# Kernel optimization log

Measured on AMD Instinct MI355X. Metric: run time of the kernel, lower is better.

## Reference

```python
import jax, jax.numpy as jnp
import numpy as np

D_IN = 1024
D_OUT = 1024
B, S = 4, 4096


def setup_inputs() -> dict:
    key = jax.random.key(0)
    ks = jax.random.split(key, 7)
    scale = 1.0 / np.sqrt(D_IN)
    return {
        "x": jax.random.normal(ks[0], (B, S, D_IN), dtype=jnp.float32),
        "Wq": jax.random.uniform(ks[1], (D_IN, D_OUT), jnp.float32, -scale, scale),
        "bq": jax.random.uniform(ks[2], (D_OUT,), jnp.float32, -scale, scale),
        "Wk": jax.random.uniform(ks[3], (D_IN, D_OUT), jnp.float32, -scale, scale),
        "bk": jax.random.uniform(ks[4], (D_OUT,), jnp.float32, -scale, scale),
        "Wv": jax.random.uniform(ks[5], (D_IN, D_OUT), jnp.float32, -scale, scale),
        "bv": jax.random.uniform(ks[6], (D_OUT,), jnp.float32, -scale, scale),
    }


def reference(x, Wq, bq, Wk, bk, Wv, bv):
    # x: [B,S,d_in]
    q = jnp.einsum("bsd,de->bse", x, Wq) + bq  # [B,S,d_out]
    k = jnp.einsum("bsd,de->bse", x, Wk) + bk
    v = jnp.einsum("bsd,de->bse", x, Wv) + bv
    scores = jnp.einsum("bqe,bke->bqk", q, k) / jnp.sqrt(jnp.float32(D_OUT))  # [B,S,S]
    attn = jax.nn.softmax(scores, axis=2)
    return jnp.einsum("bqk,bke->bqe", attn, v)  # [B,S,d_out]
```

## Files before the change

kernel.cpp:

```cpp
#include <hip/hip_runtime.h>
#include <hip/hip_bf16.h>
#include <cstdint>

#define SEQ 4096
#define NB 4
#define DIM 1024
#define MTOT (NB * SEQ)
constexpr size_t EL = (size_t)MTOT * DIM;

using u16x8  = __attribute__((ext_vector_type(8))) unsigned short;
using bf16x8 = __attribute__((ext_vector_type(8))) __bf16;
using f32x4  = __attribute__((ext_vector_type(4))) float;

__device__ __forceinline__ unsigned short f2bf(float f) {
  return __builtin_bit_cast(unsigned short, __float2bfloat16(f));
}

__device__ __forceinline__ void gload16(const unsigned short* g, unsigned short* l) {
  __builtin_amdgcn_global_load_lds(
      (const __attribute__((address_space(1))) unsigned int*)g,
      (__attribute__((address_space(3))) unsigned int*)l, 16, 0, 0);
}
__device__ __forceinline__ void stage_half(const unsigned short* gsrc, size_t ld,
                                           unsigned short* ldst) {
  gload16(gsrc, ldst);
  gload16(gsrc + 64 * ld, ldst + 64 * 64);
}

#define BAR()   __builtin_amdgcn_s_barrier()
#define FENCE() asm volatile("" ::: "memory")

__global__ __launch_bounds__(256) void prep(const float* __restrict__ x,
                                            unsigned short* __restrict__ xb,
                                            const float* __restrict__ bq,
                                            const float* __restrict__ bk,
                                            const float* __restrict__ bv,
                                            float* __restrict__ bc,
                                            float* __restrict__ l) {
  const size_t gid = (size_t)blockIdx.x * 256 + threadIdx.x;
  const size_t i = gid * 4;
  float4 v = *(const float4*)(x + i);
  ushort4 o;
  o.x = f2bf(v.x); o.y = f2bf(v.y); o.z = f2bf(v.z); o.w = f2bf(v.w);
  *(ushort4*)(xb + i) = o;
  if (gid < MTOT) l[gid] = 0.f;
  if (gid < 3 * DIM)
    bc[gid] = gid < DIM ? bq[gid] : gid < 2 * DIM ? bk[gid - DIM] : bv[gid - 2 * DIM];
}

__global__ __launch_bounds__(256) void transpose_w3(const float* __restrict__ Wq,
                                                    const float* __restrict__ Wk,
                                                    const float* __restrict__ Wv,
                                                    unsigned short* __restrict__ WT) {
  const float* W = blockIdx.z == 0 ? Wq : blockIdx.z == 1 ? Wk : Wv;
  unsigned short* O = WT + (size_t)blockIdx.z * DIM * DIM;
  __shared__ float tile[32][33];
  const int tx = threadIdx.x, ty = threadIdx.y;
  const int d0 = blockIdx.y * 32, e0 = blockIdx.x * 32;
#pragma unroll
  for (int j = 0; j < 32; j += 8)
    tile[ty + j][tx] = W[(size_t)(d0 + ty + j) * DIM + e0 + tx];
  __syncthreads();
#pragma unroll
  for (int j = 0; j < 32; j += 8)
    O[(size_t)(e0 + ty + j) * DIM + d0 + tx] = f2bf(tile[tx][ty + j]);
}

enum { EPI_QKV = 0, EPI_EXP = 1, EPI_PV = 2 };

template <int EPI>
__device__ __forceinline__ void gemm_body(
    const unsigned short* __restrict__ A, const unsigned short* __restrict__ B,
    void* __restrict__ C, const float* __restrict__ bias, float* __restrict__ lsum,
    int K, int lda, int ldb, int ldc, float scale,
    int row0, int col0, int bz, long sA, long sB, long sC) {
  __shared__ unsigned short sm[2][2][256 * 64];
  const int t    = threadIdx.x;
  const int lane = t & 63;
  const int wave = t >> 6;
  const int wm   = wave >> 2;
  const int wn   = wave & 3;
  const int fr   = lane & 15;
  const int g    = lane >> 4;
  const int xr   = (fr & 7) << 4;

  const unsigned short* Ab = A + (size_t)bz * (size_t)sA;
  const unsigned short* Bb = B + (size_t)bz * (size_t)sB;

  const int srow = t >> 3;
  const int scol = ((((t & 7) << 4) ^ ((srow & 7) << 4)) >> 1);
  const unsigned short* gA = Ab + (size_t)(row0 + srow) * (size_t)lda + scol;
  const unsigned short* gB = Bb + (size_t)(col0 + srow) * (size_t)ldb + scol;

  const int arow = wm * 128 + fr;
  const int brow = wn * 64 + fr;
  const int c0 = (((g << 4)) ^ xr) >> 1;
  const int c1 = ((64 | (g << 4)) ^ xr) >> 1;

  f32x4 acc[8][4];
  const f32x4 z4 = {0.f, 0.f, 0.f, 0.f};
#pragma unroll
  for (int i = 0; i < 8; ++i)
#pragma unroll
    for (int j = 0; j < 4; ++j) acc[i][j] = z4;

  const int nt = K >> 6;

  stage_half(gA, lda, &sm[0][0][wave * 512]);
  stage_half(gA + 128 * (size_t)lda, lda, &sm[0][0][8192 + wave * 512]);
  stage_half(gB, ldb, &sm[0][1][wave * 512]);
  stage_half(gB + 128 * (size_t)ldb, ldb, &sm[0][1][8192 + wave * 512]);
  if (nt > 1) {
    stage_half(gB + 64, ldb, &sm[1][1][wave * 512]);
    stage_half(gB + 128 * (size_t)ldb + 64, ldb, &sm[1][1][8192 + wave * 512]);
    stage_half(gA + 64, lda, &sm[1][0][wave * 512]);
    asm volatile("s_waitcnt vmcnt(6)" ::: "memory");
  } else {
    asm volatile("s_waitcnt vmcnt(0)" ::: "memory");
  }
  BAR(); FENCE();

  bf16x8 a0[4][2], a1[4][2], b0[2][2], b1[2][2];

  for (int kt = 0; kt < nt; ++kt) {
    const int p = kt & 1;
    const unsigned short* As  = sm[p][0];
    const unsigned short* Bs2 = sm[p][1];

#pragma unroll
    for (int mi = 0; mi < 4; ++mi) {
      a0[mi][0] = *(const bf16x8*)(As + (arow + mi * 16) * 64 + c0);
      a0[mi][1] = *(const bf16x8*)(As + (arow + mi * 16) * 64 + c1);
    }
#pragma unroll
    for (int ni = 0; ni < 2; ++ni) {
      b0[ni][0] = *(const bf16x8*)(Bs2 + (brow + ni * 16) * 64 + c0);
      b0[ni][1] = *(const bf16x8*)(Bs2 + (brow + ni * 16) * 64 + c1);
    }
    if (kt + 1 < nt)
      stage_half(gA + 128 * (size_t)lda + (size_t)(kt + 1) * 64, lda,
                 &sm[p ^ 1][0][8192 + wave * 512]);
    FENCE(); BAR(); FENCE();
    __builtin_amdgcn_s_setprio(1);
#pragma unroll
    for (int mi = 0; mi < 4; ++mi)
#pragma unroll
      for (int ni = 0; ni < 2; ++ni) {
        acc[mi][ni] = __builtin_amdgcn_mfma_f32_16x16x32_bf16(a0[mi][0], b0[ni][0], acc[mi][ni], 0, 0, 0);
        acc[mi][ni] = __builtin_amdgcn_mfma_f32_16x16x32_bf16(a0[mi][1], b0[ni][1], acc[mi][ni], 0, 0, 0);
      }
    __builtin_amdgcn_s_setprio(0);
    FENCE(); BAR(); FENCE();

#pragma unroll
    for (int ni = 0; ni < 2; ++ni) {
      b1[ni][0] = *(const bf16x8*)(Bs2 + (brow + (ni + 2) * 16) * 64 + c0);
      b1[ni][1] = *(const bf16x8*)(Bs2 + (brow + (ni + 2) * 16) * 64 + c1);
    }
    FENCE(); BAR(); FENCE();
    __builtin_amdgcn_s_setprio(1);
#pragma unroll
    for (int mi = 0; mi < 4; ++mi)
#pragma unroll
      for (int ni = 0; ni < 2; ++ni) {
        acc[mi][ni + 2] = __builtin_amdgcn_mfma_f32_16x16x32_bf16(a0[mi][0], b1[ni][0], acc[mi][ni + 2], 0, 0, 0);
        acc[mi][ni + 2] = __builtin_amdgcn_mfma_f32_16x16x32_bf16(a0[mi][1], b1[ni][1], acc[mi][ni + 2], 0, 0, 0);
      }
    __builtin_amdgcn_s_setprio(0);
    FENCE(); BAR(); FENCE();

#pragma unroll
    for (int mi = 0; mi < 4; ++mi) {
      a1[mi][0] = *(const bf16x8*)(As + (arow + (mi + 4) * 16) * 64 + c0);
      a1[mi][1] = *(const bf16x8*)(As + (arow + (mi + 4) * 16) * 64 + c1);
    }
    if (kt + 2 < nt)
      stage_half(gB + (size_t)(kt + 2) * 64, ldb, &sm[p][1][wave * 512]);
    FENCE(); BAR(); FENCE();
    __builtin_amdgcn_s_setprio(1);
#pragma unroll
    for (int mi = 0; mi < 4; ++mi)
#pragma unroll
      for (int ni = 0; ni < 2; ++ni) {
        acc[mi + 4][ni] = __builtin_amdgcn_mfma_f32_16x16x32_bf16(a1[mi][0], b0[ni][0], acc[mi + 4][ni], 0, 0, 0);
        acc[mi + 4][ni] = __builtin_amdgcn_mfma_f32_16x16x32_bf16(a1[mi][1], b0[ni][1], acc[mi + 4][ni], 0, 0, 0);
      }
    __builtin_amdgcn_s_setprio(0);
    FENCE(); BAR(); FENCE();

    if (kt + 2 < nt) {
      stage_half(gB + 128 * (size_t)ldb + (size_t)(kt + 2) * 64, ldb,
                 &sm[p][1][8192 + wave * 512]);
      stage_half(gA + (size_t)(kt + 2) * 64, lda, &sm[p][0][wave * 512]);
      asm volatile("s_waitcnt vmcnt(6)" ::: "memory");
    } else {
      asm volatile("s_waitcnt vmcnt(0)" ::: "memory");
    }
    FENCE(); BAR(); FENCE();
    __builtin_amdgcn_s_setprio(1);
#pragma unroll
    for (int mi = 0; mi < 4; ++mi)
#pragma unroll
      for (int ni = 0; ni < 2; ++ni) {
        acc[mi + 4][ni + 2] = __builtin_amdgcn_mfma_f32_16x16x32_bf16(a1[mi][0], b1[ni][0], acc[mi + 4][ni + 2], 0, 0, 0);
        acc[mi + 4][ni + 2] = __builtin_amdgcn_mfma_f32_16x16x32_bf16(a1[mi][1], b1[ni][1], acc[mi + 4][ni + 2], 0, 0, 0);
      }
    __builtin_amdgcn_s_setprio(0);
    FENCE(); BAR(); FENCE();
  }

  char* Lb = (char*)&sm[0][0][0];
  const int rb = (lane >> 4) * 4;

  if constexpr (EPI == EPI_QKV) {
    const int which = col0 >> 10;
    const int lc0   = col0 & 1023;
    unsigned short* Co = (unsigned short*)C + (size_t)which * EL;
    if (which < 2) {
      float bb[4];
#pragma unroll
      for (int ni = 0; ni < 4; ++ni) bb[ni] = bias[col0 + wn * 64 + ni * 16 + fr];
#pragma unroll
      for (int mi = 0; mi < 8; ++mi) {
        const int r0 = wm * 128 + mi * 16 + rb;
#pragma unroll
        for (int ni = 0; ni < 4; ++ni) {
          const int c = wn * 64 + ni * 16 + fr;
#pragma unroll
          for (int j = 0; j < 4; ++j) {
            const int r = r0 + j;
            *(unsigned short*)(Lb + r * 512 + ((c * 2) ^ ((r & 7) << 4))) =
                f2bf(acc[mi][ni][j] + bb[ni]);
          }
        }
      }
      __syncthreads();
#pragma unroll 4
      for (int i = 0; i < 16; ++i) {
        const int G = i * 512 + t;
        const int r = G >> 5, c16 = G & 31;
        u16x8 v = *(const u16x8*)(Lb + r * 512 + ((c16 * 16) ^ ((r & 7) << 4)));
        *(u16x8*)(Co + (size_t)(row0 + r) * DIM + lc0 + c16 * 8) = v;
      }
    } else {
#pragma unroll
      for (int ni = 0; ni < 4; ++ni) {
        const int c = wn * 64 + ni * 16 + fr;
        const float bb = bias[col0 + c];
#pragma unroll
        for (int mi = 0; mi < 8; ++mi) {
          const int r0 = wm * 128 + mi * 16 + rb;
          ushort4 pk;
          pk.x = f2bf(acc[mi][ni][0] + bb);
          pk.y = f2bf(acc[mi][ni][1] + bb);
          pk.z = f2bf(acc[mi][ni][2] + bb);
          pk.w = f2bf(acc[mi][ni][3] + bb);
          *(ushort4*)(Lb + c * 512 + ((r0 * 2) ^ ((c & 7) << 4))) = pk;
        }
      }
      __syncthreads();
#pragma unroll 4
      for (int i = 0; i < 16; ++i) {
        const int G = i * 512 + t;
        const int e = G >> 5, m16 = G & 31;
        u16x8 v = *(const u16x8*)(Lb + e * 512 + ((m16 * 16) ^ ((e & 7) << 4)));
        *(u16x8*)(Co + (size_t)(lc0 + e) * MTOT + row0 + m16 * 8) = v;
      }
    }
  } else if constexpr (EPI == EPI_EXP) {
#pragma unroll
    for (int mi = 0; mi < 8; ++mi)
#pragma unroll
      for (int ni = 0; ni < 4; ++ni)
#pragma unroll
        for (int j = 0; j < 4; ++j)
          acc[mi][ni][j] = exp2f(acc[mi][ni][j] * scale);

#pragma unroll
    for (int mi = 0; mi < 8; ++mi)
#pragma unroll
      for (int j = 0; j < 4; ++j) {
        float s = acc[mi][0][j] + acc[mi][1][j] + acc[mi][2][j] + acc[mi][3][j];
        s += __shfl_xor(s, 1);
        s += __shfl_xor(s, 2);
        s += __shfl_xor(s, 4);
        s += __shfl_xor(s, 8);
        if (fr == 0)
          atomicAdd(&lsum[(size_t)bz * SEQ + row0 + wm * 128 + mi * 16 + rb + j], s);
      }

#pragma unroll
    for (int mi = 0; mi < 8; ++mi) {
      const int r0 = wm * 128 + mi * 16 + rb;
#pragma unroll
      for (int ni = 0; ni < 4; ++ni) {
        const int c = wn * 64 + ni * 16 + fr;
#pragma unroll
        for (int j = 0; j < 4; ++j) {
          const int r = r0 + j;
          *(unsigned short*)(Lb + r * 512 + ((c * 2) ^ ((r & 7) << 4))) =
              f2bf(acc[mi][ni][j]);
        }
      }
    }
    __syncthreads();
    unsigned short* Co = (unsigned short*)C + (size_t)bz * (size_t)sC;
#pragma unroll 4
    for (int i = 0; i < 16; ++i) {
      const int G = i * 512 + t;
      const int r = G >> 5, c16 = G & 31;
      u16x8 v = *(const u16x8*)(Lb + r * 512 + ((c16 * 16) ^ ((r & 7) << 4)));
      *(u16x8*)(Co + (size_t)(row0 + r) * (size_t)ldc + col0 + c16 * 8) = v;
    }
  } else {
    float* Co = (float*)C + (size_t)bz * (size_t)sC;
#pragma unroll
    for (int h = 0; h < 2; ++h) {
      if (h) __syncthreads();
      if (wm == h) {
#pragma unroll
        for (int mi = 0; mi < 8; ++mi) {
          const int r0 = mi * 16 + rb;
#pragma unroll
          for (int ni = 0; ni < 4; ++ni) {
            const int c = wn * 64 + ni * 16 + fr;
#pragma unroll
            for (int j = 0; j < 4; ++j) {
              const int r = r0 + j;
              *(float*)(Lb + r * 1024 + ((c * 4) ^ ((r & 7) << 4))) = acc[mi][ni][j];
            }
          }
        }
      }
      __syncthreads();
#pragma unroll 4
      for (int i = 0; i < 16; ++i) {
        const int G = i * 512 + t;
        const int r = G >> 6, c4 = G & 63;
        f32x4 v = *(const f32x4*)(Lb + r * 1024 + ((c4 * 16) ^ ((r & 7) << 4)));
        const size_t grow = (size_t)row0 + h * 128 + r;
        const float inv = 1.0f / lsum[(size_t)bz * SEQ + grow];
        v *= inv;
        *(f32x4*)(Co + grow * (size_t)ldc + col0 + c4 * 4) = v;
      }
    }
  }
}

__global__ __launch_bounds__(512, 2) void gemm_qkv(
    const unsigned short* __restrict__ A, const unsigned short* __restrict__ B,
    unsigned short* __restrict__ C, const float* __restrict__ bcat) {
  gemm_body<EPI_QKV>(A, B, C, bcat, nullptr, DIM, DIM, DIM, DIM, 1.f,
                     (int)blockIdx.x * 256, (int)blockIdx.y * 256, 0, 0, 0, 0);
}

__global__ __launch_bounds__(512, 2) void gemm_exp(
    const unsigned short* __restrict__ A, const unsigned short* __restrict__ B,
    unsigned short* __restrict__ C, float* __restrict__ lsum) {
  gemm_body<EPI_EXP>(A, B, C, nullptr, lsum, DIM, DIM, DIM, SEQ, 0.04508422f,
                     (int)blockIdx.x * 256, (int)blockIdx.y * 256, (int)blockIdx.z,
                     (long)SEQ * DIM, (long)SEQ * DIM, (long)SEQ * SEQ);
}

__global__ __launch_bounds__(512, 2) void gemm_pv(
    const unsigned short* __restrict__ A, const unsigned short* __restrict__ B,
    float* __restrict__ C, float* __restrict__ lsum) {
  const int flat = (int)blockIdx.x +
                   (int)gridDim.x * ((int)blockIdx.y + (int)gridDim.y * (int)blockIdx.z);
  const int nf  = (flat & 7) * 32 + (flat >> 3);
  const int b   = nf >> 6;
  const int rc  = nf & 63;
  const int row = rc >> 2, col = rc & 3;
  gemm_body<EPI_PV>(A, B, C, nullptr, lsum, SEQ, SEQ, MTOT, DIM, 1.f,
                    row * 256, col * 256, b,
                    (long)SEQ * SEQ, (long)SEQ, (long)SEQ * DIM);
}

extern "C" void kernel_launch(void* const* d_in, const int* in_sizes, int n_in,
                              void* d_out, int out_size, void* d_ws, size_t ws_size,
                              hipStream_t stream) {
  (void)in_sizes; (void)n_in; (void)out_size; (void)ws_size;
  const float* x  = (const float*)d_in[0];
  const float* Wq = (const float*)d_in[1];
  const float* bq = (const float*)d_in[2];
  const float* Wk = (const float*)d_in[3];
  const float* bk = (const float*)d_in[4];
  const float* Wv = (const float*)d_in[5];
  const float* bv = (const float*)d_in[6];
  float* out = (float*)d_out;

  const size_t SALL = (size_t)NB * SEQ * SEQ;
  unsigned short* Q  = (unsigned short*)d_ws;
  unsigned short* Km = Q + EL;
  unsigned short* VT = Km + EL;
  unsigned short* Sb = VT + EL;
  unsigned short* WT = Sb + SALL;
  float*          l  = (float*)(WT + (size_t)3 * DIM * DIM);
  float*          bc = l + MTOT;
  unsigned short* xb = Sb;

  prep<<<dim3(EL / 1024), dim3(256), 0, stream>>>(x, xb, bq, bk, bv, bc, l);
  transpose_w3<<<dim3(32, 32, 3), dim3(32, 8), 0, stream>>>(Wq, Wk, Wv, WT);

  gemm_qkv<<<dim3(MTOT / 256, 3 * DIM / 256), 512, 0, stream>>>(xb, WT, Q, bc);

  gemm_exp<<<dim3(SEQ / 256, SEQ / 256, NB), 512, 0, stream>>>(Q, Km, Sb, l);

  gemm_pv<<<dim3(DIM / 256, SEQ / 256, NB), 512, 0, stream>>>(Sb, VT, out, l);
}
```

Before: 401.9 us.

## Merge prep kernels and make GEMM blocks loop over multiple output tiles

```diff
diff --git a/kernel.cpp b/kernel.cpp
--- a/kernel.cpp
+++ b/kernel.cpp
@@ -30,40 +30,42 @@
 #define BAR()   __builtin_amdgcn_s_barrier()
 #define FENCE() asm volatile("" ::: "memory")
 
-__global__ __launch_bounds__(256) void prep(const float* __restrict__ x,
-                                            unsigned short* __restrict__ xb,
-                                            const float* __restrict__ bq,
-                                            const float* __restrict__ bk,
-                                            const float* __restrict__ bv,
-                                            float* __restrict__ bc,
-                                            float* __restrict__ l) {
-  const size_t gid = (size_t)blockIdx.x * 256 + threadIdx.x;
-  const size_t i = gid * 4;
-  float4 v = *(const float4*)(x + i);
-  ushort4 o;
-  o.x = f2bf(v.x); o.y = f2bf(v.y); o.z = f2bf(v.z); o.w = f2bf(v.w);
-  *(ushort4*)(xb + i) = o;
-  if (gid < MTOT) l[gid] = 0.f;
-  if (gid < 3 * DIM)
-    bc[gid] = gid < DIM ? bq[gid] : gid < 2 * DIM ? bk[gid - DIM] : bv[gid - 2 * DIM];
-}
-
-__global__ __launch_bounds__(256) void transpose_w3(const float* __restrict__ Wq,
-                                                    const float* __restrict__ Wk,
-                                                    const float* __restrict__ Wv,
-                                                    unsigned short* __restrict__ WT) {
-  const float* W = blockIdx.z == 0 ? Wq : blockIdx.z == 1 ? Wk : Wv;
-  unsigned short* O = WT + (size_t)blockIdx.z * DIM * DIM;
+__global__ __launch_bounds__(256) void prep_all(
+    const float* __restrict__ x, unsigned short* __restrict__ xb,
+    const float* __restrict__ Wq, const float* __restrict__ Wk,
+    const float* __restrict__ Wv, unsigned short* __restrict__ WT,
+    const float* __restrict__ bq, const float* __restrict__ bk,
+    const float* __restrict__ bv, float* __restrict__ bc,
+    float* __restrict__ l) {
   __shared__ float tile[32][33];
-  const int tx = threadIdx.x, ty = threadIdx.y;
-  const int d0 = blockIdx.y * 32, e0 = blockIdx.x * 32;
-#pragma unroll
-  for (int j = 0; j < 32; j += 8)
-    tile[ty + j][tx] = W[(size_t)(d0 + ty + j) * DIM + e0 + tx];
-  __syncthreads();
-#pragma unroll
-  for (int j = 0; j < 32; j += 8)
-    O[(size_t)(e0 + ty + j) * DIM + d0 + tx] = f2bf(tile[tx][ty + j]);
+  const int bid = (int)blockIdx.x;
+  const int t = threadIdx.x;
+  if (bid < (int)(EL / 1024)) {
+    const size_t gid = (size_t)bid * 256 + t;
+    const size_t i = gid * 4;
+    float4 v = *(const float4*)(x + i);
+    ushort4 o;
+    o.x = f2bf(v.x); o.y = f2bf(v.y); o.z = f2bf(v.z); o.w = f2bf(v.w);
+    *(ushort4*)(xb + i) = o;
+    if (gid < MTOT) l[gid] = 0.f;
+    if (gid < 3 * DIM)
+      bc[gid] = gid < DIM ? bq[gid] : gid < 2 * DIM ? bk[gid - DIM] : bv[gid - 2 * DIM];
+  } else {
+    const int wb = bid - (int)(EL / 1024);
+    const int z = wb >> 10;
+    const float* W = z == 0 ? Wq : z == 1 ? Wk : Wv;
+    unsigned short* O = WT + (size_t)z * DIM * DIM;
+    const int rem = wb & 1023;
+    const int e0 = (rem & 31) * 32, d0 = (rem >> 5) * 32;
+    const int tx = t & 31, ty = t >> 5;
+#pragma unroll
+    for (int j = 0; j < 32; j += 8)
+      tile[ty + j][tx] = W[(size_t)(d0 + ty + j) * DIM + e0 + tx];
+    __syncthreads();
+#pragma unroll
+    for (int j = 0; j < 32; j += 8)
+      O[(size_t)(e0 + ty + j) * DIM + d0 + tx] = f2bf(tile[tx][ty + j]);
+  }
 }
 
 enum { EPI_QKV = 0, EPI_EXP = 1, EPI_PV = 2 };
@@ -84,6 +86,8 @@
   const int g    = lane >> 4;
   const int xr   = (fr & 7) << 4;
 
+  __syncthreads();
+
   const unsigned short* Ab = A + (size_t)bz * (size_t)sA;
   const unsigned short* Bb = B + (size_t)bz * (size_t)sB;
 
@@ -350,16 +354,25 @@
 __global__ __launch_bounds__(512, 2) void gemm_qkv(
     const unsigned short* __restrict__ A, const unsigned short* __restrict__ B,
     unsigned short* __restrict__ C, const float* __restrict__ bcat) {
-  gemm_body<EPI_QKV>(A, B, C, bcat, nullptr, DIM, DIM, DIM, DIM, 1.f,
-                     (int)blockIdx.x * 256, (int)blockIdx.y * 256, 0, 0, 0, 0);
+  const int row = (int)blockIdx.x;
+  const int c   = (int)blockIdx.y;
+#pragma unroll 1
+  for (int which = 0; which < 3; ++which)
+    gemm_body<EPI_QKV>(A, B, C, bcat, nullptr, DIM, DIM, DIM, DIM, 1.f,
+                       row * 256, which * 1024 + c * 256, 0, 0, 0, 0);
 }
 
 __global__ __launch_bounds__(512, 2) void gemm_exp(
     const unsigned short* __restrict__ A, const unsigned short* __restrict__ B,
-    unsigned short* __restrict__ C, float* __restrict__ lsum) {
-  gemm_body<EPI_EXP>(A, B, C, nullptr, lsum, DIM, DIM, DIM, SEQ, 0.04508422f,
-                     (int)blockIdx.x * 256, (int)blockIdx.y * 256, (int)blockIdx.z,
-                     (long)SEQ * DIM, (long)SEQ * DIM, (long)SEQ * SEQ);
+    unsigned short* __restrict__ C, float* __restrict__ lsum, int zoff) {
+  const int row = (int)blockIdx.x;
+  const int cp  = (int)blockIdx.y;
+  const int bz  = (int)blockIdx.z + zoff;
+#pragma unroll 1
+  for (int cc = 0; cc < 2; ++cc)
+    gemm_body<EPI_EXP>(A, B, C, nullptr, lsum, DIM, DIM, DIM, SEQ, 0.04508422f,
+                       row * 256, (cp * 2 + cc) * 256, bz,
+                       (long)SEQ * DIM, (long)SEQ * DIM, (long)SEQ * SEQ);
 }
 
 __global__ __launch_bounds__(512, 2) void gemm_pv(
@@ -399,12 +412,13 @@
   float*          bc = l + MTOT;
   unsigned short* xb = Sb;
 
-  prep<<<dim3(EL / 1024), dim3(256), 0, stream>>>(x, xb, bq, bk, bv, bc, l);
-  transpose_w3<<<dim3(32, 32, 3), dim3(32, 8), 0, stream>>>(Wq, Wk, Wv, WT);
-
-  gemm_qkv<<<dim3(MTOT / 256, 3 * DIM / 256), 512, 0, stream>>>(xb, WT, Q, bc);
-
-  gemm_exp<<<dim3(SEQ / 256, SEQ / 256, NB), 512, 0, stream>>>(Q, Km, Sb, l);
-
-  gemm_pv<<<dim3(DIM / 256, SEQ / 256, NB), 512, 0, stream>>>(Sb, VT, out, l);
-}
+  prep_all<<<dim3(EL / 1024 + 3072), dim3(256), 0, stream>>>(
+      x, xb, Wq, Wk, Wv, WT, bq, bk, bv, bc, l);
+
+  gemm_qkv<<<dim3(64, 4), 512, 0, stream>>>(xb, WT, Q, bc);
+
+  gemm_exp<<<dim3(16, 8, 2), 512, 0, stream>>>(Q, Km, Sb, l, 0);
+  gemm_exp<<<dim3(16, 8, 2), 512, 0, stream>>>(Q, Km, Sb, l, 2);
+
+  gemm_pv<<<dim3(4, 16, 4), 512, 0, stream>>>(Sb, VT, out, l);
+}
```

Result: slower. 472.5 us (+17.6%).
